# Kernel tuning notes

Measured on AMD Instinct MI355X. Metric: run time of the kernel, lower is better.

The kernel has to match this reference:

```python
import jax, jax.numpy as jnp
import numpy as np


def _chamfer(samp_pc, ref_pc):
    """Squared-L2 chamfer: returns (cost_p1_p2 [B,N], cost_p2_p1 [B,M]).

    samp_pc: [B, N, 3], ref_pc: [B, M, 3]
    """
    s2 = jnp.sum(samp_pc * samp_pc, axis=-1)  # [B, N]
    r2 = jnp.sum(ref_pc * ref_pc, axis=-1)    # [B, M]
    cross = jnp.einsum('bnd,bmd->bnm', samp_pc, ref_pc)  # [B, N, M]
    d2 = s2[:, :, None] + r2[:, None, :] - 2.0 * cross   # [B, N, M]
    d2 = jnp.maximum(d2, 0.0)  # numerical floor
    cost_p1_p2 = jnp.min(d2, axis=2)  # [B, N] nearest ref for each samp point
    cost_p2_p1 = jnp.min(d2, axis=1)  # [B, M] nearest samp for each ref point
    return cost_p1_p2, cost_p2_p1


def setup_inputs() -> dict:
    key = jax.random.key(0)
    k1, k2 = jax.random.split(key)
    B, N, M = 16, 2048, 8192
    ref_pc = jax.random.normal(k1, (B, M, 3), dtype=jnp.float32)
    samp_pc = jax.random.normal(k2, (B, N, 3), dtype=jnp.float32)
    return {"ref_pc": ref_pc, "samp_pc": samp_pc}


def reference(ref_pc, samp_pc):
    cost_p1_p2, cost_p2_p1 = _chamfer(samp_pc, ref_pc)
    cd_p = (jnp.sqrt(cost_p1_p2).mean(axis=1) + jnp.sqrt(cost_p2_p1).mean(axis=1)) / 2.0
    cd_t = cost_p1_p2.mean(axis=1) + cost_p2_p1.mean(axis=1)
    return (cd_p, cd_t)
```

## Files before the change

kernel.cpp:

```cpp
#include <hip/hip_runtime.h>
#include <math.h>

#define BB 16
#define NN 2048
#define MM 8192

#define BLK 256
#define QSPL 4
#define NQ (NN / QSPL)
#define CTS (NQ / 32)

typedef __attribute__((ext_vector_type(8))) short short8;
typedef __attribute__((ext_vector_type(16))) float f32x16;

union U16 { uint4 u; short8 s; };

static __device__ __forceinline__ unsigned short f2bf(float f) {
    unsigned int u = __float_as_uint(f);
    unsigned int r = (u + 0x7FFFu + ((u >> 16) & 1u)) >> 16;
    return (unsigned short)r;
}
static __device__ __forceinline__ float bf2f(unsigned short h) {
    return __uint_as_float(((unsigned int)h) << 16);
}

static __device__ __forceinline__ void pack5(const float a5[5], const int ord[6],
                                             unsigned int uu[16]) {
    unsigned short h[3][5];
#pragma unroll
    for (int j = 0; j < 5; ++j) {
        float v = a5[j];
        h[0][j] = f2bf(v); float r1 = v - bf2f(h[0][j]);
        h[1][j] = f2bf(r1); float r2 = r1 - bf2f(h[1][j]);
        h[2][j] = f2bf(r2);
    }
    unsigned short K[32];
#pragma unroll
    for (int f = 0; f < 2; ++f) {
#pragma unroll
        for (int p2 = 0; p2 < 3; ++p2)
#pragma unroll
            for (int j2 = 0; j2 < 5; ++j2)
                K[f * 16 + p2 * 5 + j2] = h[ord[f * 3 + p2]][j2];
        K[f * 16 + 15] = 0;
    }
#pragma unroll
    for (int t = 0; t < 16; ++t)
        uu[t] = (unsigned int)K[2 * t] | ((unsigned int)K[2 * t + 1] << 16);
}

#define DPP_MIN(v, CTRL)                                                      \
    v = fminf(v, __uint_as_float((unsigned)__builtin_amdgcn_update_dpp(       \
                     0, (int)__float_as_uint(v), CTRL, 0xF, 0xF, true)))
#define SWZ16_MIN(v)                                                          \
    v = fminf(v, __uint_as_float((unsigned)__builtin_amdgcn_ds_swizzle(       \
                     (int)__float_as_uint(v), 0x401F)))


__global__ void __launch_bounds__(BLK, 4) sweep_kernel(const float* __restrict__ ref,
                                                       const float* __restrict__ samp,
                                                       unsigned int* __restrict__ ws2,
                                                       unsigned int* __restrict__ ws1) {
    __shared__ uint4 Qf[4][NQ];
    __shared__ unsigned int qMin[NQ];

    const int b = blockIdx.x;
    const int m0 = blockIdx.y * 256;
    const int q0 = blockIdx.z * NQ;
    const int tid = threadIdx.x;
    const int w = tid >> 6;
    const int l = tid & 63;
    const int p = l & 31;
    const int kh = l >> 5;

    const int ordR[6] = {0, 0, 1, 0, 2, 1};
    const int ordQ[6] = {0, 1, 0, 2, 0, 1};

    U16 a0f0, a0f1, a1f0, a1f1;
    {
        const float* r0 = ref + ((size_t)(b * MM + m0 + w * 64 + p)) * 3;
        float x = r0[0], y = r0[1], z = r0[2];
        float a5[5] = {-2.f * x, -2.f * y, -2.f * z, fmaf(x, x, fmaf(y, y, z * z)), 1.f};
        unsigned int uu[16];
        pack5(a5, ordR, uu);
        a0f0.u = kh ? make_uint4(uu[4], uu[5], uu[6], uu[7])
                    : make_uint4(uu[0], uu[1], uu[2], uu[3]);
        a0f1.u = kh ? make_uint4(uu[12], uu[13], uu[14], uu[15])
                    : make_uint4(uu[8], uu[9], uu[10], uu[11]);
        const float* r1 = r0 + 32 * 3;
        x = r1[0]; y = r1[1]; z = r1[2];
        float a6[5] = {-2.f * x, -2.f * y, -2.f * z, fmaf(x, x, fmaf(y, y, z * z)), 1.f};
        pack5(a6, ordR, uu);
        a1f0.u = kh ? make_uint4(uu[4], uu[5], uu[6], uu[7])
                    : make_uint4(uu[0], uu[1], uu[2], uu[3]);
        a1f1.u = kh ? make_uint4(uu[12], uu[13], uu[14], uu[15])
                    : make_uint4(uu[8], uu[9], uu[10], uu[11]);
    }

#pragma unroll
    for (int k2 = 0; k2 < NQ / BLK; ++k2) {
        const int q = k2 * BLK + tid;
        const float* s0 = samp + ((size_t)(b * NN + q0 + q)) * 3;
        float x = s0[0], y = s0[1], z = s0[2];
        float a5[5] = {x, y, z, 1.f, fmaf(x, x, fmaf(y, y, z * z))};
        unsigned int uu[16];
        pack5(a5, ordQ, uu);
        Qf[0][q] = make_uint4(uu[0], uu[1], uu[2], uu[3]);
        Qf[1][q] = make_uint4(uu[4], uu[5], uu[6], uu[7]);
        Qf[2][q] = make_uint4(uu[8], uu[9], uu[10], uu[11]);
        Qf[3][q] = make_uint4(uu[12], uu[13], uu[14], uu[15]);
    }
    qMin[tid] = 0x7F7F7F7Fu;
    qMin[tid + BLK] = 0x7F7F7F7Fu;
    __syncthreads();

    float run0[16], run1[16];
#pragma unroll
    for (int j = 0; j < 16; ++j) { run0[j] = INFINITY; run1[j] = INFINITY; }

    const f32x16 fz = {0.f, 0.f, 0.f, 0.f, 0.f, 0.f, 0.f, 0.f,
                       0.f, 0.f, 0.f, 0.f, 0.f, 0.f, 0.f, 0.f};

#pragma unroll 2
    for (int ct = 0; ct < CTS; ++ct) {
        const int q = ct * 32 + p;
        U16 b0, b1;
        b0.u = Qf[kh][q];
        b1.u = Qf[2 + kh][q];
        f32x16 d0 = __builtin_amdgcn_mfma_f32_32x32x16_bf16(a0f0.s, b0.s, fz, 0, 0, 0);
        d0 = __builtin_amdgcn_mfma_f32_32x32x16_bf16(a0f1.s, b1.s, d0, 0, 0, 0);
        f32x16 d1 = __builtin_amdgcn_mfma_f32_32x32x16_bf16(a1f0.s, b0.s, fz, 0, 0, 0);
        d1 = __builtin_amdgcn_mfma_f32_32x32x16_bf16(a1f1.s, b1.s, d1, 0, 0, 0);
#pragma unroll
        for (int j = 0; j < 16; ++j) {
            run0[j] = fminf(run0[j], d0[j]);
            run1[j] = fminf(run1[j], d1[j]);
        }
        float tv[8];
#pragma unroll
        for (int k = 0; k < 8; ++k) tv[k] = fminf(d0[k], d0[k + 8]);
#pragma unroll
        for (int k = 0; k < 8; ++k) tv[k] = fminf(tv[k], fminf(d1[k], d1[k + 8]));
#pragma unroll
        for (int k = 0; k < 4; ++k) tv[k] = fminf(tv[k], tv[k + 4]);
        float t = fminf(fminf(tv[0], tv[2]), fminf(tv[1], tv[3]));
        atomicMin(&qMin[q], __float_as_uint(fmaxf(t, 0.f)));
    }
    __syncthreads();

    unsigned int* w1 = ws1 + (size_t)b * NN + q0;
    atomicMin(&w1[tid], qMin[tid]);
    atomicMin(&w1[tid + BLK], qMin[tid + BLK]);

#pragma unroll
    for (int j = 0; j < 16; ++j) {
        DPP_MIN(run0[j], 0xB1);  DPP_MIN(run0[j], 0x4E);
        DPP_MIN(run0[j], 0x141); DPP_MIN(run0[j], 0x140);
        SWZ16_MIN(run0[j]);
        DPP_MIN(run1[j], 0xB1);  DPP_MIN(run1[j], 0x4E);
        DPP_MIN(run1[j], 0x141); DPP_MIN(run1[j], 0x140);
        SWZ16_MIN(run1[j]);
    }
    float out = 0.f;
#pragma unroll
    for (int j = 0; j < 16; ++j) { if (p == j)      out = run0[j]; }
#pragma unroll
    for (int j = 0; j < 16; ++j) { if (p == 16 + j) out = run1[j]; }
    const int t2 = p >> 4, j4 = p & 15;
    const int row = t2 * 32 + (j4 & 3) + ((j4 >> 2) << 3) + 4 * kh;
    atomicMin(&ws2[(size_t)b * MM + m0 + w * 64 + row],
              __float_as_uint(fmaxf(out, 0.f)));
}

#define BLKR 1024
__global__ void __launch_bounds__(BLKR) reduce_kernel(const unsigned int* __restrict__ ws1,
                                                      const unsigned int* __restrict__ ws2,
                                                      float* __restrict__ out) {
    const int b = blockIdx.x;
    const int tid = threadIdx.x;
    const int lane = tid & 63;
    const int wv = tid >> 6;

    float sd1 = 0.f, sr1 = 0.f, sd2 = 0.f, sr2 = 0.f;
#pragma unroll
    for (int i = tid; i < NN; i += BLKR) {
        float v = __uint_as_float(ws1[(size_t)b * NN + i]);
        sd1 += v;
        sr1 += sqrtf(v);
    }
#pragma unroll
    for (int i = tid; i < MM; i += BLKR) {
        float v = __uint_as_float(ws2[(size_t)b * MM + i]);
        sd2 += v;
        sr2 += sqrtf(v);
    }
#pragma unroll
    for (int s = 32; s > 0; s >>= 1) {
        sd1 += __shfl_xor(sd1, s);
        sr1 += __shfl_xor(sr1, s);
        sd2 += __shfl_xor(sd2, s);
        sr2 += __shfl_xor(sr2, s);
    }

    __shared__ float4 red[BLKR / 64];
    if (lane == 0) red[wv] = make_float4(sd1, sr1, sd2, sr2);
    __syncthreads();
    if (tid == 0) {
        float4 acc = red[0];
#pragma unroll
        for (int w = 1; w < BLKR / 64; ++w) {
            acc.x += red[w].x; acc.y += red[w].y;
            acc.z += red[w].z; acc.w += red[w].w;
        }
        out[b]      = (acc.y * (1.0f / NN) + acc.w * (1.0f / MM)) * 0.5f;
        out[BB + b] = acc.x * (1.0f / NN) + acc.z * (1.0f / MM);
    }
}

extern "C" void kernel_launch(void* const* d_in, const int* in_sizes, int n_in,
                              void* d_out, int out_size, void* d_ws, size_t ws_size,
                              hipStream_t stream) {
    const float* ref  = (const float*)d_in[0];
    const float* samp = (const float*)d_in[1];
    float* out = (float*)d_out;

    unsigned int* ws2 = (unsigned int*)d_ws;
    unsigned int* ws1 = ws2 + (size_t)BB * MM;

    hipMemsetAsync(d_ws, 0x7F, ((size_t)BB * MM + (size_t)BB * NN) * sizeof(unsigned int), stream);

    dim3 gs(BB, MM / 256, QSPL);
    sweep_kernel<<<gs, BLK, 0, stream>>>(ref, samp, ws2, ws1);

    reduce_kernel<<<BB, BLKR, 0, stream>>>(ws1, ws2, out);
}
```

Baseline: 87.29 us.

## Fuse final reduction into sweep kernel via last-block ticket counter

Drops the separate reduce kernel launch. Each sweep block increments a per-batch atomic ticket after its atomicMin writes, and the last block to arrive for a batch reads the workspace and computes the means and sqrt sums. This removes one kernel launch and its dependency gap. In exchange every block pays a threadfence and an atomic, and the final reduction per batch runs on one 256-thread block instead of 1024 threads.

```diff
diff --git a/kernel.cpp b/kernel.cpp
--- a/kernel.cpp
+++ b/kernel.cpp
@@ -9,6 +9,8 @@
 #define QSPL 4
 #define NQ (NN / QSPL)
 #define CTS (NQ / 32)
+#define BPB ((MM / 256) * QSPL)
+#define TICKET_LAST (0x7F7F7F7Fu + (unsigned)BPB - 1u)
 
 typedef __attribute__((ext_vector_type(8))) short short8;
 typedef __attribute__((ext_vector_type(16))) float f32x16;
@@ -60,9 +62,13 @@
 __global__ void __launch_bounds__(BLK, 4) sweep_kernel(const float* __restrict__ ref,
                                                        const float* __restrict__ samp,
                                                        unsigned int* __restrict__ ws2,
-                                                       unsigned int* __restrict__ ws1) {
+                                                       unsigned int* __restrict__ ws1,
+                                                       unsigned int* __restrict__ cnt,
+                                                       float* __restrict__ out) {
     __shared__ uint4 Qf[4][NQ];
     __shared__ unsigned int qMin[NQ];
+    __shared__ unsigned int ticket_s;
+    __shared__ float4 red2[4];
 
     const int b = blockIdx.x;
     const int m0 = blockIdx.y * 256;
@@ -161,38 +167,36 @@
         DPP_MIN(run1[j], 0x141); DPP_MIN(run1[j], 0x140);
         SWZ16_MIN(run1[j]);
     }
-    float out = 0.f;
-#pragma unroll
-    for (int j = 0; j < 16; ++j) { if (p == j)      out = run0[j]; }
-#pragma unroll
-    for (int j = 0; j < 16; ++j) { if (p == 16 + j) out = run1[j]; }
+    float outv = 0.f;
+#pragma unroll
+    for (int j = 0; j < 16; ++j) { if (p == j)      outv = run0[j]; }
+#pragma unroll
+    for (int j = 0; j < 16; ++j) { if (p == 16 + j) outv = run1[j]; }
     const int t2 = p >> 4, j4 = p & 15;
     const int row = t2 * 32 + (j4 & 3) + ((j4 >> 2) << 3) + 4 * kh;
     atomicMin(&ws2[(size_t)b * MM + m0 + w * 64 + row],
-              __float_as_uint(fmaxf(out, 0.f)));
-}
-
-#define BLKR 1024
-__global__ void __launch_bounds__(BLKR) reduce_kernel(const unsigned int* __restrict__ ws1,
-                                                      const unsigned int* __restrict__ ws2,
-                                                      float* __restrict__ out) {
-    const int b = blockIdx.x;
-    const int tid = threadIdx.x;
-    const int lane = tid & 63;
-    const int wv = tid >> 6;
+              __float_as_uint(fmaxf(outv, 0.f)));
+
+    __threadfence();
+    __syncthreads();
+    if (tid == 0)
+        ticket_s = __hip_atomic_fetch_add(&cnt[b], 1u, __ATOMIC_ACQ_REL,
+                                          __HIP_MEMORY_SCOPE_AGENT);
+    __syncthreads();
+    if (ticket_s != TICKET_LAST) return;
 
     float sd1 = 0.f, sr1 = 0.f, sd2 = 0.f, sr2 = 0.f;
-#pragma unroll
-    for (int i = tid; i < NN; i += BLKR) {
-        float v = __uint_as_float(ws1[(size_t)b * NN + i]);
-        sd1 += v;
-        sr1 += sqrtf(v);
-    }
-#pragma unroll
-    for (int i = tid; i < MM; i += BLKR) {
-        float v = __uint_as_float(ws2[(size_t)b * MM + i]);
-        sd2 += v;
-        sr2 += sqrtf(v);
+    for (int i = tid; i < NN; i += BLK) {
+        unsigned int u = __hip_atomic_load(&ws1[(size_t)b * NN + i],
+                                           __ATOMIC_RELAXED, __HIP_MEMORY_SCOPE_AGENT);
+        float v = fmaxf(__uint_as_float(u), 0.f);
+        sd1 += v; sr1 += sqrtf(v);
+    }
+    for (int i = tid; i < MM; i += BLK) {
+        unsigned int u = __hip_atomic_load(&ws2[(size_t)b * MM + i],
+                                           __ATOMIC_RELAXED, __HIP_MEMORY_SCOPE_AGENT);
+        float v = fmaxf(__uint_as_float(u), 0.f);
+        sd2 += v; sr2 += sqrtf(v);
     }
 #pragma unroll
     for (int s = 32; s > 0; s >>= 1) {
@@ -201,16 +205,14 @@
         sd2 += __shfl_xor(sd2, s);
         sr2 += __shfl_xor(sr2, s);
     }
-
-    __shared__ float4 red[BLKR / 64];
-    if (lane == 0) red[wv] = make_float4(sd1, sr1, sd2, sr2);
+    if (l == 0) red2[w] = make_float4(sd1, sr1, sd2, sr2);
     __syncthreads();
     if (tid == 0) {
-        float4 acc = red[0];
-#pragma unroll
-        for (int w = 1; w < BLKR / 64; ++w) {
-            acc.x += red[w].x; acc.y += red[w].y;
-            acc.z += red[w].z; acc.w += red[w].w;
+        float4 acc = red2[0];
+#pragma unroll
+        for (int ww = 1; ww < 4; ++ww) {
+            acc.x += red2[ww].x; acc.y += red2[ww].y;
+            acc.z += red2[ww].z; acc.w += red2[ww].w;
         }
         out[b]      = (acc.y * (1.0f / NN) + acc.w * (1.0f / MM)) * 0.5f;
         out[BB + b] = acc.x * (1.0f / NN) + acc.z * (1.0f / MM);
@@ -226,11 +228,12 @@
 
     unsigned int* ws2 = (unsigned int*)d_ws;
     unsigned int* ws1 = ws2 + (size_t)BB * MM;
-
-    hipMemsetAsync(d_ws, 0x7F, ((size_t)BB * MM + (size_t)BB * NN) * sizeof(unsigned int), stream);
+    unsigned int* cnt = ws1 + (size_t)BB * NN;
+
+    hipMemsetAsync(d_ws, 0x7F,
+                   ((size_t)BB * MM + (size_t)BB * NN + BB) * sizeof(unsigned int),
+                   stream);
 
     dim3 gs(BB, MM / 256, QSPL);
-    sweep_kernel<<<gs, BLK, 0, stream>>>(ref, samp, ws2, ws1);
-
-    reduce_kernel<<<BB, BLKR, 0, stream>>>(ws1, ws2, out);
-}
+    sweep_kernel<<<gs, BLK, 0, stream>>>(ref, samp, ws2, ws1, cnt, out);
+}
```

New measurement: 227.8 us. +160.9%, slower.

## Precompute bf16-split operands in a prep kernel and stream Q tiles via global_load_lds

Applied to the files above, without the earlier changes.

Adds a prep kernel that packs the three-way bf16 splits of every sample and reference point once into workspace and also initializes the min buffers, which replaces the memset. Before, each sweep block recomputed this packing, and the grid repeats it 32x for samples and 4x for refs. The sweep kernel now copies the prepacked Q tile straight into LDS with global_load_lds and loads its A fragments from global memory. In exchange it adds an extra launch and global traffic for the packed buffers, and it depends on the workspace being large enough.

```diff
diff --git a/kernel.cpp b/kernel.cpp
--- a/kernel.cpp
+++ b/kernel.cpp
@@ -9,6 +9,8 @@
 #define QSPL 4
 #define NQ (NN / QSPL)
 #define CTS (NQ / 32)
+#define PN (BB * NN)
+#define PTOT (BB * (NN + MM))
 
 typedef __attribute__((ext_vector_type(8))) short short8;
 typedef __attribute__((ext_vector_type(16))) float f32x16;
@@ -47,6 +49,13 @@
 #pragma unroll
     for (int t = 0; t < 16; ++t)
         uu[t] = (unsigned int)K[2 * t] | ((unsigned int)K[2 * t + 1] << 16);
+}
+
+static __device__ __forceinline__ void glds16(const uint4* g, uint4* l) {
+    __builtin_amdgcn_global_load_lds(
+        (const __attribute__((address_space(1))) unsigned int*)g,
+        (__attribute__((address_space(3))) unsigned int*)l,
+        16, 0, 0);
 }
 
 #define DPP_MIN(v, CTRL)                                                      \
@@ -57,11 +66,50 @@
                      (int)__float_as_uint(v), 0x401F)))
 
 
-__global__ void __launch_bounds__(BLK, 4) sweep_kernel(const float* __restrict__ ref,
-                                                       const float* __restrict__ samp,
+__global__ void __launch_bounds__(BLK) prep_kernel(const float* __restrict__ ref,
+                                                   const float* __restrict__ samp,
+                                                   unsigned short* __restrict__ Qpk,
+                                                   unsigned short* __restrict__ Rpk,
+                                                   unsigned int* __restrict__ wsinit) {
+    const int i = blockIdx.x * BLK + threadIdx.x;
+    wsinit[i] = 0x7F7F7F7Fu;
+
+    const int ordR[6] = {0, 0, 1, 0, 2, 1};
+    const int ordQ[6] = {0, 1, 0, 2, 0, 1};
+
+    if (i < PN) {
+        const float* s0 = samp + (size_t)i * 3;
+        float x = s0[0], y = s0[1], z = s0[2];
+        float a5[5] = {x, y, z, 1.f, fmaf(x, x, fmaf(y, y, z * z))};
+        unsigned int uu[16];
+        pack5(a5, ordQ, uu);
+        const int bq = i >> 11, n = i & (NN - 1);
+        const int g = n >> 9, qin = n & (NQ - 1);
+        uint4* Q4 = (uint4*)Qpk + ((size_t)(bq * QSPL + g) * 4) * NQ + qin;
+        Q4[0 * NQ] = make_uint4(uu[0], uu[1], uu[2], uu[3]);
+        Q4[1 * NQ] = make_uint4(uu[4], uu[5], uu[6], uu[7]);
+        Q4[2 * NQ] = make_uint4(uu[8], uu[9], uu[10], uu[11]);
+        Q4[3 * NQ] = make_uint4(uu[12], uu[13], uu[14], uu[15]);
+    } else {
+        const int j = i - PN;
+        const float* r0 = ref + (size_t)j * 3;
+        float x = r0[0], y = r0[1], z = r0[2];
+        float a5[5] = {-2.f * x, -2.f * y, -2.f * z, fmaf(x, x, fmaf(y, y, z * z)), 1.f};
+        unsigned int uu[16];
+        pack5(a5, ordR, uu);
+        uint4* R4 = (uint4*)Rpk + (size_t)j * 4;
+        R4[0] = make_uint4(uu[0], uu[1], uu[2], uu[3]);
+        R4[1] = make_uint4(uu[4], uu[5], uu[6], uu[7]);
+        R4[2] = make_uint4(uu[8], uu[9], uu[10], uu[11]);
+        R4[3] = make_uint4(uu[12], uu[13], uu[14], uu[15]);
+    }
+}
+
+__global__ void __launch_bounds__(BLK, 4) sweep_kernel(const unsigned short* __restrict__ Qpk,
+                                                       const unsigned short* __restrict__ Rpk,
                                                        unsigned int* __restrict__ ws2,
                                                        unsigned int* __restrict__ ws1) {
-    __shared__ uint4 Qf[4][NQ];
+    __shared__ uint4 Qf[4 * NQ];
     __shared__ unsigned int qMin[NQ];
 
     const int b = blockIdx.x;
@@ -73,43 +121,16 @@
     const int p = l & 31;
     const int kh = l >> 5;
 
-    const int ordR[6] = {0, 0, 1, 0, 2, 1};
-    const int ordQ[6] = {0, 1, 0, 2, 0, 1};
-
+    const uint4* qsrc = (const uint4*)Qpk + ((size_t)(b * QSPL + blockIdx.z) * 4) * NQ;
+#pragma unroll
+    for (int k = 0; k < (4 * NQ) / BLK; ++k)
+        glds16(qsrc + k * BLK + tid, Qf + k * BLK + tid);
+
+    const uint4* R4 = (const uint4*)Rpk + ((size_t)(b * MM + m0 + w * 64 + p)) * 4;
     U16 a0f0, a0f1, a1f0, a1f1;
-    {
-        const float* r0 = ref + ((size_t)(b * MM + m0 + w * 64 + p)) * 3;
-        float x = r0[0], y = r0[1], z = r0[2];
-        float a5[5] = {-2.f * x, -2.f * y, -2.f * z, fmaf(x, x, fmaf(y, y, z * z)), 1.f};
-        unsigned int uu[16];
-        pack5(a5, ordR, uu);
-        a0f0.u = kh ? make_uint4(uu[4], uu[5], uu[6], uu[7])
-                    : make_uint4(uu[0], uu[1], uu[2], uu[3]);
-        a0f1.u = kh ? make_uint4(uu[12], uu[13], uu[14], uu[15])
-                    : make_uint4(uu[8], uu[9], uu[10], uu[11]);
-        const float* r1 = r0 + 32 * 3;
-        x = r1[0]; y = r1[1]; z = r1[2];
-        float a6[5] = {-2.f * x, -2.f * y, -2.f * z, fmaf(x, x, fmaf(y, y, z * z)), 1.f};
-        pack5(a6, ordR, uu);
-        a1f0.u = kh ? make_uint4(uu[4], uu[5], uu[6], uu[7])
-                    : make_uint4(uu[0], uu[1], uu[2], uu[3]);
-        a1f1.u = kh ? make_uint4(uu[12], uu[13], uu[14], uu[15])
-                    : make_uint4(uu[8], uu[9], uu[10], uu[11]);
-    }
-
-#pragma unroll
-    for (int k2 = 0; k2 < NQ / BLK; ++k2) {
-        const int q = k2 * BLK + tid;
-        const float* s0 = samp + ((size_t)(b * NN + q0 + q)) * 3;
-        float x = s0[0], y = s0[1], z = s0[2];
-        float a5[5] = {x, y, z, 1.f, fmaf(x, x, fmaf(y, y, z * z))};
-        unsigned int uu[16];
-        pack5(a5, ordQ, uu);
-        Qf[0][q] = make_uint4(uu[0], uu[1], uu[2], uu[3]);
-        Qf[1][q] = make_uint4(uu[4], uu[5], uu[6], uu[7]);
-        Qf[2][q] = make_uint4(uu[8], uu[9], uu[10], uu[11]);
-        Qf[3][q] = make_uint4(uu[12], uu[13], uu[14], uu[15]);
-    }
+    a0f0.u = R4[kh];         a0f1.u = R4[2 + kh];
+    a1f0.u = R4[128 + kh];   a1f1.u = R4[128 + 2 + kh];
+
     qMin[tid] = 0x7F7F7F7Fu;
     qMin[tid + BLK] = 0x7F7F7F7Fu;
     __syncthreads();
@@ -125,8 +146,8 @@
     for (int ct = 0; ct < CTS; ++ct) {
         const int q = ct * 32 + p;
         U16 b0, b1;
-        b0.u = Qf[kh][q];
-        b1.u = Qf[2 + kh][q];
+        b0.u = Qf[kh * NQ + q];
+        b1.u = Qf[(2 + kh) * NQ + q];
         f32x16 d0 = __builtin_amdgcn_mfma_f32_32x32x16_bf16(a0f0.s, b0.s, fz, 0, 0, 0);
         d0 = __builtin_amdgcn_mfma_f32_32x32x16_bf16(a0f1.s, b1.s, d0, 0, 0, 0);
         f32x16 d1 = __builtin_amdgcn_mfma_f32_32x32x16_bf16(a1f0.s, b0.s, fz, 0, 0, 0);
@@ -161,15 +182,15 @@
         DPP_MIN(run1[j], 0x141); DPP_MIN(run1[j], 0x140);
         SWZ16_MIN(run1[j]);
     }
-    float out = 0.f;
-#pragma unroll
-    for (int j = 0; j < 16; ++j) { if (p == j)      out = run0[j]; }
-#pragma unroll
-    for (int j = 0; j < 16; ++j) { if (p == 16 + j) out = run1[j]; }
+    float outv = 0.f;
+#pragma unroll
+    for (int j = 0; j < 16; ++j) { if (p == j)      outv = run0[j]; }
+#pragma unroll
+    for (int j = 0; j < 16; ++j) { if (p == 16 + j) outv = run1[j]; }
     const int t2 = p >> 4, j4 = p & 15;
     const int row = t2 * 32 + (j4 & 3) + ((j4 >> 2) << 3) + 4 * kh;
     atomicMin(&ws2[(size_t)b * MM + m0 + w * 64 + row],
-              __float_as_uint(fmaxf(out, 0.f)));
+              __float_as_uint(fmaxf(outv, 0.f)));
 }
 
 #define BLKR 1024
@@ -226,11 +247,13 @@
 
     unsigned int* ws2 = (unsigned int*)d_ws;
     unsigned int* ws1 = ws2 + (size_t)BB * MM;
-
-    hipMemsetAsync(d_ws, 0x7F, ((size_t)BB * MM + (size_t)BB * NN) * sizeof(unsigned int), stream);
+    unsigned short* Qpk = (unsigned short*)(ws1 + (size_t)BB * NN);
+    unsigned short* Rpk = Qpk + (size_t)BB * NN * 32;
+
+    prep_kernel<<<PTOT / BLK, BLK, 0, stream>>>(ref, samp, Qpk, Rpk, ws2);
 
     dim3 gs(BB, MM / 256, QSPL);
-    sweep_kernel<<<gs, BLK, 0, stream>>>(ref, samp, ws2, ws1);
+    sweep_kernel<<<gs, BLK, 0, stream>>>(Qpk, Rpk, ws2, ws1);
 
     reduce_kernel<<<BB, BLKR, 0, stream>>>(ws1, ws2, out);
 }
```

Measured after the change: 94.87 us. 1.09x slower.
